# Performance work log

Measured on AMD Instinct MI355X. Metric: run time of the kernel, lower is better.

The kernel has to match this reference:

```python
import jax, jax.numpy as jnp
import numpy as np
from jax import lax

# ---- configuration (matches init_kwargs) ----
B, C_DATA, C_FEAT, H, W = 2, 8, 8, 160, 160
K = 7                      # number of soft nearest neighbors
PS, STRIDE, WIN = 10, 5, 15
FEAT, C_EMB = 64, 8
N1 = (H - PS) // STRIDE + 1   # 31, no padding needed
N2 = (W - PS) // STRIDE + 1   # 31
NEG_INF = -1e9


def _conv3(x, w, b):
    y = lax.conv_general_dilated(x, w, (1, 1), 'SAME',
                                 dimension_numbers=('NCHW', 'OIHW', 'NCHW'))
    return y + b[None, :, None, None]


def _cnn(x, w1, b1, w2, b2, w3, b3):
    # depth-3 DnCNN-style net: conv-relu-conv-relu-conv (bn=False, lastact=linear)
    h = jax.nn.relu(_conv3(x, w1, b1))
    h = jax.nn.relu(_conv3(h, w2, b2))
    return _conv3(h, w3, b3)


def _im2patch(x):
    # x: [b,c,H,W] -> [b,n1,n2,c*PS*PS]; patch flattened channel-major (c,p1,p2)
    ii = jnp.arange(N1)[:, None] * STRIDE + jnp.arange(PS)[None, :]  # [n1,PS]
    jj = jnp.arange(N2)[:, None] * STRIDE + jnp.arange(PS)[None, :]  # [n2,PS]
    p = x[:, :, ii[:, None, :, None], jj[None, :, None, :]]  # [b,c,n1,n2,PS,PS]
    p = jnp.transpose(p, (0, 2, 3, 1, 4, 5))
    return p.reshape(p.shape[0], N1, N2, -1)


def _n3block(x_data, x_faet, ew1, eb1, ew2, eb2, ew3, eb3,
             tw1, tb1, tw2, tb2, tw3, tb3):
    xe = _cnn(x_faet, ew1, eb1, ew2, eb2, ew3, eb3)      # [b,8,H,W] embeddings
    log_temp = _cnn(x_faet, tw1, tb1, tw2, tb2, tw3, tb3)  # [b,1,H,W]

    ye = _im2patch(xe)                        # [b,n1,n2,E]; queries == database
    yp = _im2patch(x_data)                    # [b,n1,n2,F]
    lt = _im2patch(log_temp).mean(-1)         # scalar log-temp per patch
    temp = jnp.exp(lt)[..., None]             # [b,n1,n2,1] (temp_bias = 1)

    S = min(WIN, N1, N2)
    R = S // 2
    base1 = jnp.clip(jnp.arange(N1) - R, 0, N1 - S)   # clamped window top-left
    base2 = jnp.clip(jnp.arange(N2) - R, 0, N2 - S)
    offs = jnp.stack(jnp.meshgrid(jnp.arange(S), jnp.arange(S), indexing='ij'),
                     axis=-1).reshape(-1, 2)          # [S*S,2]
    i1, i2 = jnp.arange(N1), jnp.arange(N2)
    yn = jnp.sum(ye * ye, axis=-1)            # [b,n1,n2] squared norms

    @jax.checkpoint
    def dist_step(carry, off):
        j1 = base1 + off[0]
        j2 = base2 + off[1]
        xs = ye[:, j1][:, :, j2]              # [b,n1,n2,E] candidate embedding
        xn = yn[:, j1][:, :, j2]
        dot = jnp.einsum('bije,bije->bij', ye, xs)
        d = yn + xn - 2.0 * dot               # squared euclidean distance
        self_m = (j1 == i1)[:, None] & (j2 == i2)[None, :]
        return carry, (d, self_m)

    _, (D, selfm) = lax.scan(dist_step, None, offs)
    D = jnp.moveaxis(D, 0, -1)                # [b,n1,n2,O], O=S*S
    selfm = jnp.moveaxis(selfm, 0, -1)        # [n1,n2,O]

    logits = -D / temp
    logits = jnp.where(selfm, NEG_INF, logits)   # exclude_self

    # continuous deterministic top-k (N3Net): w_j = softmax(a); a += log(1 - w_j)
    ws = []
    for _ in range(K):
        wgt = jax.nn.softmax(logits, axis=-1)
        ws.append(wgt)
        logits = logits + jnp.log1p(-jnp.minimum(wgt, 1.0 - 1e-6))
    Wk = jnp.stack(ws, axis=-1)               # [b,n1,n2,O,K]

    @jax.checkpoint
    def agg_step(z, args):
        off, wk = args                        # wk: [b,n1,n2,K]
        j1 = base1 + off[0]
        j2 = base2 + off[1]
        ys = yp[:, j1][:, :, j2]              # [b,n1,n2,F]
        return z + wk[..., :, None] * ys[..., None, :], None

    z0 = jnp.zeros(yp.shape[:3] + (K, yp.shape[-1]), yp.dtype)
    z, _ = lax.scan(agg_step, z0, (offs, jnp.moveaxis(Wk, 3, 0)))
    z = z - yp[..., None, :]                  # residue=True
    out_p = jnp.concatenate([yp[..., None, :], z], axis=3)  # [b,n1,n2,K+1,F]

    # fold patch volumes back to image, averaging overlaps
    b = out_p.shape[0]
    C = (K + 1) * C_DATA
    out_p = out_p.reshape(b, N1, N2, K + 1, C_DATA, PS, PS)
    out_p = jnp.transpose(out_p, (0, 3, 4, 1, 2, 5, 6)).reshape(b, C, N1, N2, PS, PS)
    rows = jnp.arange(N1)[:, None] * STRIDE + jnp.arange(PS)[None, :]
    cols = jnp.arange(N2)[:, None] * STRIDE + jnp.arange(PS)[None, :]
    lin = (rows[:, None, :, None] * W + cols[None, :, None, :]).reshape(-1)
    vals = out_p.reshape(b, C, -1)
    img = jnp.zeros((b, C, H * W), out_p.dtype).at[:, :, lin].add(vals)
    cnt = jnp.zeros((H * W,), out_p.dtype).at[lin].add(1.0)
    return (img / cnt).reshape(b, C, H, W)


def setup_inputs() -> dict:
    key = jax.random.key(0)
    ks = jax.random.split(key, 8)
    f32 = jnp.float32
    wn = lambda k, s: jax.random.normal(k, s, f32) * 0.05
    return dict(
        x_data=jax.random.normal(ks[0], (B, C_DATA, H, W), f32),
        x_faet=jax.random.normal(ks[1], (B, C_FEAT, H, W), f32),
        ew1=wn(ks[2], (FEAT, C_FEAT, 3, 3)), eb1=jnp.zeros((FEAT,), f32),
        ew2=wn(ks[3], (FEAT, FEAT, 3, 3)), eb2=jnp.zeros((FEAT,), f32),
        ew3=wn(ks[4], (C_EMB, FEAT, 3, 3)), eb3=jnp.zeros((C_EMB,), f32),
        tw1=wn(ks[5], (FEAT, C_FEAT, 3, 3)), tb1=jnp.zeros((FEAT,), f32),
        tw2=wn(ks[6], (FEAT, FEAT, 3, 3)), tb2=jnp.zeros((FEAT,), f32),
        tw3=wn(ks[7], (1, FEAT, 3, 3)), tb3=jnp.zeros((1,), f32),
    )


def reference(x_data, x_faet, ew1, eb1, ew2, eb2, ew3, eb3,
              tw1, tb1, tw2, tb2, tw3, tb3):
    return _n3block(x_data, x_faet, ew1, eb1, ew2, eb2, ew3, eb3,
                    tw1, tb1, tw2, tb2, tw3, tb3)
```

## Files before the change

### kernel.cpp

```cpp
#include <hip/hip_runtime.h>
#include <math.h>

#define BN 2
#define HH 160
#define WW 160
#define CDATA 8
#define PS 10
#define STR 5
#define N1 31
#define N2 31
#define NSITE (N1*N2)
#define SITES (BN*NSITE)
#define SWIN 15
#define NOFF 225
#define KK 7
#define EDIM 800
#define NPIX 25600
#define LP 40
#define LP2 72
#define KP 480
#define COLP 992
#define GP 34
#define KSPLIT 5
#define GRAMBLKS (BN*N1*2*KSPLIT)
#define YNTBLKS ((SITES+3)/4)

typedef __attribute__((ext_vector_type(8))) short s8v;
typedef __attribute__((ext_vector_type(8))) unsigned short u8v;
typedef __attribute__((ext_vector_type(4))) unsigned short u4v;
typedef __attribute__((ext_vector_type(4))) float f4v;

__device__ __forceinline__ unsigned short f2bf(float f) {
    unsigned u = __float_as_uint(f);
    return (unsigned short)((u + 0x7FFFu + ((u >> 16) & 1u)) >> 16);
}
__device__ __forceinline__ float bf2f(unsigned short h) {
    return __uint_as_float(((unsigned)h) << 16);
}

__global__ __launch_bounds__(256) void prep_k(const float* __restrict__ ew2,
                                              const float* __restrict__ tw2,
                                              const float* __restrict__ ew1,
                                              const float* __restrict__ tw1,
                                              const float* __restrict__ ew3,
                                              const float* __restrict__ tw3,
                                              unsigned short* __restrict__ wp,
                                              unsigned short* __restrict__ wp1,
                                              unsigned short* __restrict__ wp3) {
    int blk = blockIdx.x;
    int t = threadIdx.x;
    if (blk < 288) {
        int idx = blk * 256 + t;
        int which = idx / (64 * 576); int r = idx % (64 * 576);
        int n = r / 576, k = r % 576;
        int p = k / 64, c = k % 64;
        const float* w = which ? tw2 : ew2;
        wp[idx] = f2bf(w[(n * 64 + c) * 9 + p]);
    } else if (blk < 336) {
        int idx = (blk - 288) * 256 + t;
        if (idx < 128 * 96) {
            int n = idx / 96, k = idx % 96;
            int tap = k >> 3, c = k & 7;
            unsigned short v = 0;
            if (tap < 9) {
                const float* w = (n < 64) ? ew1 : tw1;
                v = f2bf(w[((n & 63) * 8 + c) * 9 + tap]);
            }
            wp1[idx] = v;
        }
    } else {
        int idx = (blk - 336) * 256 + t;
        if (idx < 2 * 16 * 576) {
            int which = idx / (16 * 576); int r = idx % (16 * 576);
            int n = r / 576, k = r % 576;
            int tap = k / 64, c = k % 64;
            float w = 0.f; bool lo = false;
            if (which == 0) { w = ew3[((n & 7) * 64 + c) * 9 + tap]; lo = (n >= 8); }
            else if (n < 2) { w = tw3[c * 9 + tap]; lo = (n == 1); }
            unsigned short hi = f2bf(w);
            wp3[idx] = lo ? f2bf(w - bf2f(hi)) : hi;
            if (which == 1 && n >= 2) wp3[idx] = 0;
        }
    }
}

__global__ __launch_bounds__(256) void conv1_ypt_k(const float* __restrict__ xf,
                                                   const float* __restrict__ xd,
                                                   const unsigned short* __restrict__ wp1,
                                                   const float* __restrict__ eb1,
                                                   const float* __restrict__ tb1,
                                                   unsigned short* __restrict__ h1,
                                                   unsigned short* __restrict__ ypT) {
    const int t = threadIdx.x;
    if (blockIdx.x >= 800) {
        int row = blockIdx.x - 800;
        int b = row / 800, e = row % 800;
        int cd = e & 7, pp = e >> 3;
        int pi = pp / 10, pj = pp % 10;
        const float* src = xd + ((size_t)(b * 8 + cd) * HH + pi) * WW + pj;
        unsigned short* dst = ypT + (size_t)row * COLP;
        for (int it = 0; it < 4; ++it) {
            int col = it * 256 + t;
            if (col < COLP) {
                int j1 = col >> 5, j2 = col & 31;
                unsigned short v = 0;
                if (j2 < 31) v = f2bf(src[(j1 * 5) * WW + j2 * 5]);
                dst[col] = v;
            }
        }
        return;
    }
    __shared__ unsigned short Al[128 * LP];
    __shared__ unsigned short Bl[64 * LP];
    const int m0 = blockIdx.x * 64;
    const int wv = t >> 6, lane = t & 63;
    f4v acc[2][4];
    #pragma unroll
    for (int fj = 0; fj < 2; ++fj)
        #pragma unroll
        for (int fi = 0; fi < 4; ++fi) { f4v z = {0.f,0.f,0.f,0.f}; acc[fj][fi] = z; }
    const int mp = m0 + (t >> 2);
    const int b = mp / NPIX, rp = mp % NPIX;
    const int py = rp / WW, px = rp % WW;
    for (int ks = 0; ks < 3; ++ks) {
        int tap = ks * 4 + (t & 3);
        int dy = tap / 3 - 1, dx = tap % 3 - 1;
        int yy = py + dy, xx = px + dx;
        bool ok = (tap < 9) && yy >= 0 && yy < HH && xx >= 0 && xx < WW;
        u8v bv;
        #pragma unroll
        for (int c = 0; c < 8; ++c)
            bv[c] = ok ? f2bf(xf[((size_t)(b * 8 + c)) * NPIX + yy * WW + xx]) : 0;
        __syncthreads();
        *(u8v*)(Bl + (t >> 2) * LP + (t & 3) * 8) = bv;
        #pragma unroll
        for (int it = 0; it < 2; ++it) {
            int idx = t + it * 256;
            int row = idx >> 2, seg = idx & 3;
            *(u8v*)(Al + row * LP + seg * 8) = *(const u8v*)(wp1 + row * 96 + ks * 32 + seg * 8);
        }
        __syncthreads();
        s8v af[2], bf[4];
        #pragma unroll
        for (int fj = 0; fj < 2; ++fj)
            af[fj] = *(const s8v*)((const short*)Al + (wv * 32 + fj * 16 + (lane & 15)) * LP + (lane >> 4) * 8);
        #pragma unroll
        for (int fi = 0; fi < 4; ++fi)
            bf[fi] = *(const s8v*)((const short*)Bl + (fi * 16 + (lane & 15)) * LP + (lane >> 4) * 8);
        #pragma unroll
        for (int fj = 0; fj < 2; ++fj)
            #pragma unroll
            for (int fi = 0; fi < 4; ++fi)
                acc[fj][fi] = __builtin_amdgcn_mfma_f32_16x16x32_bf16(af[fj], bf[fi], acc[fj][fi], 0, 0, 0);
    }
    #pragma unroll
    for (int fj = 0; fj < 2; ++fj) {
        int nb = wv * 32 + fj * 16 + (lane >> 4) * 4;
        float bias4[4];
        #pragma unroll
        for (int c = 0; c < 4; ++c) {
            int n = nb + c;
            bias4[c] = (n < 64) ? eb1[n] : tb1[n - 64];
        }
        #pragma unroll
        for (int fi = 0; fi < 4; ++fi) {
            int mm = m0 + fi * 16 + (lane & 15);
            ushort4 o;
            o.x = f2bf(fmaxf(acc[fj][fi][0] + bias4[0], 0.f));
            o.y = f2bf(fmaxf(acc[fj][fi][1] + bias4[1], 0.f));
            o.z = f2bf(fmaxf(acc[fj][fi][2] + bias4[2], 0.f));
            o.w = f2bf(fmaxf(acc[fj][fi][3] + bias4[3], 0.f));
            *(ushort4*)(h1 + (size_t)mm * 128 + nb) = o;
        }
    }
}

__global__ __launch_bounds__(256) void conv2_mfma_k(const unsigned short* __restrict__ h1,
                                                    const unsigned short* __restrict__ wp,
                                                    const float* __restrict__ eb2,
                                                    const float* __restrict__ tb2,
                                                    unsigned short* __restrict__ h2) {
    __shared__ unsigned short Al[64 * LP2];
    __shared__ unsigned short Bl[128 * LP2];
    const int t = threadIdx.x;
    const int which = blockIdx.y;
    const int m0 = blockIdx.x * 128;
    const int wv = t >> 6, lane = t & 63;
    f4v acc[4][2];
    #pragma unroll
    for (int nf = 0; nf < 4; ++nf)
        #pragma unroll
        for (int mf = 0; mf < 2; ++mf) { f4v z = {0.f,0.f,0.f,0.f}; acc[nf][mf] = z; }
    const unsigned short* wb = wp + (size_t)which * 64 * 576;
    const int sm = t >> 2, sq = (t & 3) * 8;
    const int mp0 = m0 + sm;
    const int b0 = mp0 / NPIX, rp0 = mp0 % NPIX;
    const int py0 = rp0 / WW, px0 = rp0 % WW;
    const int mp1 = m0 + 64 + sm;
    const int b1_ = mp1 / NPIX, rp1 = mp1 % NPIX;
    const int py1 = rp1 / WW, px1 = rp1 % WW;
    for (int p = 0; p < 9; ++p) {
        const int dy = p / 3 - 1, dx = p % 3 - 1;
        s8v av[2], bv0[2], bv1[2];
        #pragma unroll
        for (int hh = 0; hh < 2; ++hh) {
            av[hh] = *(const s8v*)(wb + sm * 576 + p * 64 + hh * 32 + sq);
            #pragma unroll
            for (int j = 0; j < 8; j++) { bv0[hh][j] = 0; bv1[hh][j] = 0; }
        }
        int yy = py0 + dy, xx = px0 + dx;
        if (yy >= 0 && yy < HH && xx >= 0 && xx < WW) {
            const short* src = (const short*)h1 + ((size_t)b0 * NPIX + yy * WW + xx) * 128 + which * 64 + sq;
            bv0[0] = *(const s8v*)src; bv0[1] = *(const s8v*)(src + 32);
        }
        yy = py1 + dy; xx = px1 + dx;
        if (yy >= 0 && yy < HH && xx >= 0 && xx < WW) {
            const short* src = (const short*)h1 + ((size_t)b1_ * NPIX + yy * WW + xx) * 128 + which * 64 + sq;
            bv1[0] = *(const s8v*)src; bv1[1] = *(const s8v*)(src + 32);
        }
        __syncthreads();
        #pragma unroll
        for (int hh = 0; hh < 2; ++hh) {
            *(s8v*)((short*)Al + sm * LP2 + hh * 32 + sq) = av[hh];
            *(s8v*)((short*)Bl + sm * LP2 + hh * 32 + sq) = bv0[hh];
            *(s8v*)((short*)Bl + (64 + sm) * LP2 + hh * 32 + sq) = bv1[hh];
        }
        __syncthreads();
        #pragma unroll
        for (int kk = 0; kk < 2; ++kk) {
            s8v af[4], bf[2];
            #pragma unroll
            for (int nf = 0; nf < 4; ++nf)
                af[nf] = *(const s8v*)((const short*)Al + (nf * 16 + (lane & 15)) * LP2 + kk * 32 + (lane >> 4) * 8);
            #pragma unroll
            for (int mf = 0; mf < 2; ++mf)
                bf[mf] = *(const s8v*)((const short*)Bl + (wv * 32 + mf * 16 + (lane & 15)) * LP2 + kk * 32 + (lane >> 4) * 8);
            #pragma unroll
            for (int nf = 0; nf < 4; ++nf)
                #pragma unroll
                for (int mf = 0; mf < 2; ++mf)
                    acc[nf][mf] = __builtin_amdgcn_mfma_f32_16x16x32_bf16(af[nf], bf[mf], acc[nf][mf], 0, 0, 0);
        }
    }
    const float* bias = which ? tb2 : eb2;
    #pragma unroll
    for (int nf = 0; nf < 4; ++nf) {
        int nb = nf * 16 + (lane >> 4) * 4;
        f4v bv4 = *(const f4v*)(bias + nb);
        #pragma unroll
        for (int mf = 0; mf < 2; ++mf) {
            int mm = m0 + wv * 32 + mf * 16 + (lane & 15);
            ushort4 o;
            o.x = f2bf(fmaxf(acc[nf][mf][0] + bv4[0], 0.f));
            o.y = f2bf(fmaxf(acc[nf][mf][1] + bv4[1], 0.f));
            o.z = f2bf(fmaxf(acc[nf][mf][2] + bv4[2], 0.f));
            o.w = f2bf(fmaxf(acc[nf][mf][3] + bv4[3], 0.f));
            *(ushort4*)(h2 + ((size_t)which * 51200 + mm) * 64 + nb) = o;
        }
    }
}

__global__ __launch_bounds__(256) void conv3_mfma_k(const unsigned short* __restrict__ h2,
                                                    const unsigned short* __restrict__ wp3,
                                                    const float* __restrict__ eb3,
                                                    const float* __restrict__ tb3,
                                                    unsigned short* __restrict__ xeH,
                                                    unsigned short* __restrict__ xeL,
                                                    float* __restrict__ splane,
                                                    float* __restrict__ ltm) {
    __shared__ unsigned short Al[16 * LP];
    __shared__ unsigned short Bl[128 * LP];
    const int t = threadIdx.x;
    const int which = blockIdx.y;
    const int m0 = blockIdx.x * 128;
    const int wv = t >> 6, lane = t & 63;
    f4v acc[2];
    { f4v z = {0.f,0.f,0.f,0.f}; acc[0] = z; acc[1] = z; }
    const unsigned short* wb = wp3 + (size_t)which * 16 * 576;
    const int sm = t >> 2, sq = (t & 3) * 8;
    const int mp0 = m0 + sm;
    const int b0 = mp0 / NPIX, rp0 = mp0 % NPIX;
    const int py0 = rp0 / WW, px0 = rp0 % WW;
    const int mp1 = m0 + 64 + sm;
    const int b1_ = mp1 / NPIX, rp1 = mp1 % NPIX;
    const int py1 = rp1 / WW, px1 = rp1 % WW;
    for (int step = 0; step < 18; ++step) {
        const int p = step >> 1, ch = (step & 1) * 32;
        const int dy = p / 3 - 1, dx = p % 3 - 1;
        s8v av;
        if (t < 64) av = *(const s8v*)(wb + (t >> 2) * 576 + p * 64 + ch + (t & 3) * 8);
        s8v bv0, bv1;
        #pragma unroll
        for (int j = 0; j < 8; j++) { bv0[j] = 0; bv1[j] = 0; }
        int yy = py0 + dy, xx = px0 + dx;
        if (yy >= 0 && yy < HH && xx >= 0 && xx < WW)
            bv0 = *(const s8v*)((const short*)h2 + ((size_t)which * 51200 + (size_t)b0 * NPIX + yy * WW + xx) * 64 + ch + sq);
        yy = py1 + dy; xx = px1 + dx;
        if (yy >= 0 && yy < HH && xx >= 0 && xx < WW)
            bv1 = *(const s8v*)((const short*)h2 + ((size_t)which * 51200 + (size_t)b1_ * NPIX + yy * WW + xx) * 64 + ch + sq);
        __syncthreads();
        if (t < 64) *(s8v*)((short*)Al + (t >> 2) * LP + (t & 3) * 8) = av;
        *(s8v*)((short*)Bl + sm * LP + sq) = bv0;
        *(s8v*)((short*)Bl + (64 + sm) * LP + sq) = bv1;
        __syncthreads();
        s8v af = *(const s8v*)((const short*)Al + (lane & 15) * LP + (lane >> 4) * 8);
        #pragma unroll
        for (int mf = 0; mf < 2; ++mf) {
            s8v bf = *(const s8v*)((const short*)Bl + (wv * 32 + mf * 16 + (lane & 15)) * LP + (lane >> 4) * 8);
            acc[mf] = __builtin_amdgcn_mfma_f32_16x16x32_bf16(af, bf, acc[mf], 0, 0, 0);
        }
    }
    #pragma unroll
    for (int mf = 0; mf < 2; ++mf) {
        int mm = m0 + wv * 32 + mf * 16 + (lane & 15);
        if (which == 0) {
            f4v hilo;
            #pragma unroll
            for (int c = 0; c < 4; ++c)
                hilo[c] = acc[mf][c] + __shfl_xor(acc[mf][c], 32);
            if (lane < 32) {
                int nb = (lane >> 4) * 4;
                u4v hs, ls;
                float ss = 0.f;
                #pragma unroll
                for (int c = 0; c < 4; ++c) {
                    float v = hilo[c] + eb3[nb + c];
                    unsigned short h = f2bf(v);
                    hs[c] = h;
                    ls[c] = f2bf(v - bf2f(h));
                    ss += v * v;
                }
                *(u4v*)(xeH + (size_t)mm * 8 + nb) = hs;
                *(u4v*)(xeL + (size_t)mm * 8 + nb) = ls;
                ss += __shfl_xor(ss, 16);
                if (lane < 16) splane[mm] = ss;
            }
        } else {
            if ((lane >> 4) == 0)
                ltm[mm] = acc[mf][0] + acc[mf][1] + tb3[0];
        }
    }
}

__global__ __launch_bounds__(256) void gram_ynt_k(const unsigned short* __restrict__ xeH,
                                                  const unsigned short* __restrict__ xeL,
                                                  const float* __restrict__ splane,
                                                  const float* __restrict__ ltm,
                                                  float* __restrict__ dotsC,
                                                  float* __restrict__ yn,
                                                  float* __restrict__ tempv) {
    if (blockIdx.x >= GRAMBLKS) {
        int wv = threadIdx.x >> 6, lane = threadIdx.x & 63;
        int wid = (blockIdx.x - GRAMBLKS) * 4 + wv;
        if (wid >= SITES) return;
        int b = wid / NSITE; int ij = wid % NSITE;
        int i1 = ij / N2, i2 = ij % N2;
        float s1 = 0.f, s2 = 0.f;
        for (int p = lane; p < 100; p += 64) {
            int rr = p / 10, q = p % 10;
            int idx = b * NPIX + (i1 * STR + rr) * WW + i2 * STR + q;
            s1 += splane[idx];
            s2 += ltm[idx];
        }
        #pragma unroll
        for (int o = 32; o; o >>= 1) { s1 += __shfl_xor(s1, o); s2 += __shfl_xor(s2, o); }
        if (lane == 0) {
            yn[wid] = s1;
            tempv[wid] = expf(s2 * (1.f / 100.f));
        }
        return;
    }
    __shared__ unsigned short AsH[32 * GP], AsL[32 * GP];
    __shared__ unsigned short BsH[256 * GP], BsL[256 * GP];
    int blk = blockIdx.x;
    int kc = blk % KSPLIT; int r = blk / KSPLIT;
    int nh = r & 1; r >>= 1;
    int b = r / N1, i1 = r % N1;
    int b1 = min(max(i1 - 7, 0), 16);
    int t = threadIdx.x;
    int wv = t >> 6, lane = t & 63;
    f4v acc[2][4];
    #pragma unroll
    for (int mt = 0; mt < 2; ++mt)
        #pragma unroll
        for (int nt = 0; nt < 4; ++nt) { f4v z = {0.f,0.f,0.f,0.f}; acc[mt][nt] = z; }
    const size_t pbase = (size_t)b * NPIX;
    for (int ks = kc * 5; ks < kc * 5 + 5; ++ks) {
        __syncthreads();
        {
            int idx = t & 127;
            int row = idx >> 2, seg = idx & 3;
            int p = ks * 4 + seg;
            int rr = p / 10, q = p - rr * 10;
            u8v v;
            #pragma unroll
            for (int u = 0; u < 8; ++u) v[u] = 0;
            if (row < 31) {
                size_t a = (pbase + (size_t)(i1 * STR + rr) * WW + row * STR + q) * 8;
                v = *(const u8v*)((t < 128 ? xeH : xeL) + a);
            }
            *(u8v*)((t < 128 ? AsH : AsL) + row * GP + seg * 8) = v;
        }
        #pragma unroll
        for (int rep = 0; rep < 8; ++rep) {
            int idx = t + rep * 256;
            int isH = idx < 1024;
            int id2 = idx & 1023;
            int row = id2 >> 2, seg = id2 & 3;
            int dj = nh * 8 + (row >> 5), j2 = row & 31;
            int p = ks * 4 + seg;
            int rr = p / 10, q = p - rr * 10;
            u8v v;
            #pragma unroll
            for (int u = 0; u < 8; ++u) v[u] = 0;
            if (dj < 15 && j2 < 31) {
                size_t a = (pbase + (size_t)((b1 + dj) * STR + rr) * WW + j2 * STR + q) * 8;
                v = *(const u8v*)((isH ? xeH : xeL) + a);
            }
            *(u8v*)((isH ? BsH : BsL) + row * GP + seg * 8) = v;
        }
        __syncthreads();
        s8v afH[2], afL[2], bfH[4], bfL[4];
        #pragma unroll
        for (int mt = 0; mt < 2; ++mt) {
            int ar = mt * 16 + (lane & 15);
            afH[mt] = *(const s8v*)((const short*)AsH + ar * GP + (lane >> 4) * 8);
            afL[mt] = *(const s8v*)((const short*)AsL + ar * GP + (lane >> 4) * 8);
        }
        #pragma unroll
        for (int nt = 0; nt < 4; ++nt) {
            int br = wv * 64 + nt * 16 + (lane & 15);
            bfH[nt] = *(const s8v*)((const short*)BsH + br * GP + (lane >> 4) * 8);
            bfL[nt] = *(const s8v*)((const short*)BsL + br * GP + (lane >> 4) * 8);
        }
        #pragma unroll
        for (int mt = 0; mt < 2; ++mt)
            #pragma unroll
            for (int nt = 0; nt < 4; ++nt) {
                acc[mt][nt] = __builtin_amdgcn_mfma_f32_16x16x32_bf16(afH[mt], bfH[nt], acc[mt][nt], 0, 0, 0);
                acc[mt][nt] = __builtin_amdgcn_mfma_f32_16x16x32_bf16(afH[mt], bfL[nt], acc[mt][nt], 0, 0, 0);
                acc[mt][nt] = __builtin_amdgcn_mfma_f32_16x16x32_bf16(afL[mt], bfH[nt], acc[mt][nt], 0, 0, 0);
            }
    }
    float* dk = dotsC + (size_t)kc * SITES * NOFF;
    #pragma unroll
    for (int mt = 0; mt < 2; ++mt) {
        int i2b = mt * 16 + (lane >> 4) * 4;
        #pragma unroll
        for (int nt = 0; nt < 4; ++nt) {
            int n = wv * 64 + nt * 16 + (lane & 15);
            int dj = nh * 8 + (n >> 5), j2 = n & 31;
            if (dj >= 15 || j2 >= 31) continue;
            #pragma unroll
            for (int c = 0; c < 4; ++c) {
                int i2 = i2b + c;
                if (i2 >= 31) continue;
                int b2 = min(max(i2 - 7, 0), 16);
                int dc = j2 - b2;
                if (dc < 0 || dc >= SWIN) continue;
                size_t site = (size_t)((b * N1 + i1) * N2 + i2);
                dk[site * NOFF + dj * SWIN + dc] = acc[mt][nt][c];
            }
        }
    }
}

__global__ __launch_bounds__(256) void softmax_awrite_k(const float* __restrict__ dotsC,
                                                        const float* __restrict__ yn,
                                                        const float* __restrict__ tempv,
                                                        unsigned short* __restrict__ Aglob) {
    __shared__ float sw[4][228];
    int wv = threadIdx.x >> 6, lane = threadIdx.x & 63;
    int wid = blockIdx.x * 4 + wv;
    bool active = (wid < SITES);
    int wids = active ? wid : (SITES - 1);
    int b = wids / NSITE; int ij = wids % NSITE;
    int i1 = ij / N2, i2 = ij % N2;
    int b1 = min(max(i1 - 7, 0), 16);
    int b2 = min(max(i2 - 7, 0), 16);
    int pglob = i2 >> 1, s = i2 & 1;
    unsigned short* Abase = Aglob + (size_t)((b * N1 + i1) * 256) * KP;
    float yns = yn[wids];
    float tvi = 1.f / tempv[wids];
    float lg[4];
    #pragma unroll
    for (int r = 0; r < 4; ++r) {
        int t = lane + 64 * r;
        lg[r] = -1e9f;
        if (t < NOFF) {
            float dot = 0.f;
            #pragma unroll
            for (int kc = 0; kc < KSPLIT; ++kc)
                dot += dotsC[((size_t)kc * SITES + wids) * NOFF + t];
            int dj = t / SWIN, dc = t % SWIN;
            int j1 = b1 + dj, j2 = b2 + dc;
            float xn = yn[(b * N1 + j1) * N2 + j2];
            float d = yns + xn - 2.f * dot;
            lg[r] = -d * tvi;
            if (j1 == i1 && j2 == i2) lg[r] = -1e9f;
        }
    }
    for (int k = 0; k < KK; ++k) {
        float m = fmaxf(fmaxf(lg[0], lg[1]), fmaxf(lg[2], lg[3]));
        #pragma unroll
        for (int o = 32; o; o >>= 1) m = fmaxf(m, __shfl_xor(m, o));
        float ex[4]; float ssum = 0.f;
        #pragma unroll
        for (int r = 0; r < 4; ++r) { ex[r] = __expf(lg[r] - m); ssum += ex[r]; }
        #pragma unroll
        for (int o = 32; o; o >>= 1) ssum += __shfl_xor(ssum, o);
        float inv = 1.f / ssum;
        #pragma unroll
        for (int r = 0; r < 4; ++r) {
            float wgt = ex[r] * inv;
            int t = lane + 64 * r;
            if (t < NOFF) sw[wv][t] = wgt;
            lg[r] += log1pf(-fminf(wgt, 1.f - 1e-6f));
        }
        __syncthreads();
        if (active && lane < 60) {
            u8v o;
            #pragma unroll
            for (int u = 0; u < 8; ++u) {
                int n = lane * 8 + u;
                int dj = n >> 5, j2 = n & 31;
                int dc = j2 - b2;
                o[u] = (j2 < 31 && dc >= 0 && dc < SWIN) ? f2bf(sw[wv][dj * SWIN + dc]) : (unsigned short)0;
            }
            int m_ = 16 * pglob + k + 7 * s;
            *(u8v*)(Abase + (size_t)m_ * KP + lane * 8) = o;
        }
        __syncthreads();
    }
    if (active && s == 0 && lane < 60) {
        u8v z;
        #pragma unroll
        for (int u = 0; u < 8; ++u) z[u] = 0;
        *(u8v*)(Abase + (size_t)(16 * pglob + 14) * KP + lane * 8) = z;
        *(u8v*)(Abase + (size_t)(16 * pglob + 15) * KP + lane * 8) = z;
        if (i2 == 30) {
            #pragma unroll
            for (int sl = 7; sl < 14; ++sl)
                *(u8v*)(Abase + (size_t)(16 * 15 + sl) * KP + lane * 8) = z;
        }
    }
}

__global__ __launch_bounds__(256) void agg_gemm_k(const unsigned short* __restrict__ Aglob,
                                                  const unsigned short* __restrict__ ypT,
                                                  unsigned short* __restrict__ zbuf) {
    __shared__ unsigned short As[128 * 40];
    __shared__ unsigned short Bs[160 * 40];
    int blk = blockIdx.x;
    int b = blk / 310; int r = blk % 310;
    int i1 = r / 10; int r2 = r % 10;
    int mh = r2 / 5, nc = r2 % 5;
    int b1 = min(max(i1 - 7, 0), 16);
    int t = threadIdx.x;
    int wv = t >> 6, lane = t & 63;
    int wm = (wv & 1) * 64, we = (wv >> 1) * 80;
    const unsigned short* Ab = Aglob + ((size_t)(b * N1 + i1) * 256 + mh * 128) * KP;
    const unsigned short* Bb = ypT + ((size_t)b * 800 + nc * 160) * COLP + b1 * 32;
    f4v accr[4][5];
    #pragma unroll
    for (int mt = 0; mt < 4; ++mt)
        #pragma unroll
        for (int et = 0; et < 5; ++et) { f4v z = {0.f,0.f,0.f,0.f}; accr[mt][et] = z; }
    for (int ks = 0; ks < 15; ++ks) {
        __syncthreads();
        #pragma unroll
        for (int it = 0; it < 2; ++it) {
            int idx = t + it * 256;
            int row = idx >> 2, seg = idx & 3;
            *(u8v*)(As + row * 40 + seg * 8) = *(const u8v*)(Ab + (size_t)row * KP + ks * 32 + seg * 8);
        }
        #pragma unroll
        for (int it = 0; it < 3; ++it) {
            int idx = t + it * 256;
            if (idx < 640) {
                int row = idx >> 2, seg = idx & 3;
                *(u8v*)(Bs + row * 40 + seg * 8) = *(const u8v*)(Bb + (size_t)row * COLP + ks * 32 + seg * 8);
            }
        }
        __syncthreads();
        s8v af[4], bf[5];
        #pragma unroll
        for (int mt = 0; mt < 4; ++mt)
            af[mt] = *(const s8v*)((const short*)As + (wm + mt * 16 + (lane & 15)) * 40 + (lane >> 4) * 8);
        #pragma unroll
        for (int et = 0; et < 5; ++et)
            bf[et] = *(const s8v*)((const short*)Bs + (we + et * 16 + (lane & 15)) * 40 + (lane >> 4) * 8);
        #pragma unroll
        for (int mt = 0; mt < 4; ++mt)
            #pragma unroll
            for (int et = 0; et < 5; ++et)
                accr[mt][et] = __builtin_amdgcn_mfma_f32_16x16x32_bf16(af[mt], bf[et], accr[mt][et], 0, 0, 0);
    }
    unsigned short* zb = zbuf + ((size_t)(b * N1 + i1) * 256 + mh * 128) * 800 + nc * 160;
    #pragma unroll
    for (int mt = 0; mt < 4; ++mt) {
        int mrow = wm + mt * 16 + (lane >> 4) * 4;
        #pragma unroll
        for (int et = 0; et < 5; ++et) {
            int ecol = we + et * 16 + (lane & 15);
            #pragma unroll
            for (int c = 0; c < 4; ++c)
                zb[(size_t)(mrow + c) * 800 + ecol] = f2bf(accr[mt][et][c]);
        }
    }
}

__global__ __launch_bounds__(256) void finalize_k(const unsigned short* __restrict__ zbuf,
                                                  const float* __restrict__ xd,
                                                  float* __restrict__ out) {
    int pid = blockIdx.x * 256 + threadIdx.x;
    if (pid >= BN * NPIX) return;
    int b = pid / NPIX, pix = pid % NPIX;
    int h = pix / WW, w_ = pix % WW;
    int lo1 = max(0, (h - 5) / 5),  hi1 = min(30, h / 5);
    int lo2 = max(0, (w_ - 5) / 5), hi2 = min(30, w_ / 5);
    float cntinv = 1.f / (float)((hi1 - lo1 + 1) * (hi2 - lo2 + 1));
    float xv[8];
    #pragma unroll
    for (int cd = 0; cd < 8; ++cd) {
        xv[cd] = xd[((size_t)(b * 8 + cd)) * NPIX + pix];
        out[((size_t)(b * 64 + cd)) * NPIX + pix] = xv[cd];
    }
    for (int k = 0; k < KK; ++k) {
        float s[8];
        #pragma unroll
        for (int cd = 0; cd < 8; ++cd) s[cd] = 0.f;
        for (int i1 = lo1; i1 <= hi1; ++i1) {
            int pi = h - 5 * i1;
            for (int i2 = lo2; i2 <= hi2; ++i2) {
                int pj = w_ - 5 * i2;
                int m = 16 * (i2 >> 1) + k + 7 * (i2 & 1);
                const unsigned short* zp = zbuf + ((size_t)(b * N1 + i1) * 256 + m) * 800 + (pi * 10 + pj) * 8;
                u8v zv = *(const u8v*)zp;
                #pragma unroll
                for (int cd = 0; cd < 8; ++cd) s[cd] += bf2f(zv[cd]);
            }
        }
        #pragma unroll
        for (int cd = 0; cd < 8; ++cd)
            out[((size_t)(b * 64 + (k + 1) * 8 + cd)) * NPIX + pix] = s[cd] * cntinv - xv[cd];
    }
}

extern "C" void kernel_launch(void* const* d_in, const int* in_sizes, int n_in,
                              void* d_out, int out_size, void* d_ws, size_t ws_size,
                              hipStream_t stream) {
    (void)in_sizes; (void)n_in; (void)out_size; (void)ws_size;
    const float* x_data = (const float*)d_in[0];
    const float* x_faet = (const float*)d_in[1];
    const float* ew1 = (const float*)d_in[2];  const float* eb1 = (const float*)d_in[3];
    const float* ew2 = (const float*)d_in[4];  const float* eb2 = (const float*)d_in[5];
    const float* ew3 = (const float*)d_in[6];  const float* eb3 = (const float*)d_in[7];
    const float* tw1 = (const float*)d_in[8];  const float* tb1 = (const float*)d_in[9];
    const float* tw2 = (const float*)d_in[10]; const float* tb2 = (const float*)d_in[11];
    const float* tw3 = (const float*)d_in[12]; const float* tb3 = (const float*)d_in[13];
    float* out = (float*)d_out;

    char* base = (char*)d_ws;
    unsigned short* h1 = (unsigned short*)(base);
    unsigned short* h2 = (unsigned short*)(base + 13107200);
    unsigned short* wp1 = (unsigned short*)(base + 13107200);
    unsigned short* wp = (unsigned short*)(base + 26214400);
    float* yn    = (float*)(base + 26361856);
    float* tempv = (float*)(base + 26370048);
    unsigned short* ypT = (unsigned short*)(base + 26378240);
    unsigned short* xeH = (unsigned short*)(base + 29552640);
    unsigned short* xeL = (unsigned short*)(base + 30371840);
    float* ltm    = (float*)(base + 31191040);
    float* splane = (float*)(base + 31395840);
    unsigned short* wp3 = (unsigned short*)(base + 37546240);
    unsigned short* Aglob = (unsigned short*)(base + 29552640);
    float* dotsC = (float*)h2;
    unsigned short* zbuf = (unsigned short*)base;

    prep_k<<<408, 256, 0, stream>>>(ew2, tw2, ew1, tw1, ew3, tw3, wp, wp1, wp3);
    conv1_ypt_k<<<800 + 1600, 256, 0, stream>>>(x_faet, x_data, wp1, eb1, tb1, h1, ypT);
    conv2_mfma_k<<<dim3(400, 2), 256, 0, stream>>>(h1, wp, eb2, tb2, h2);
    conv3_mfma_k<<<dim3(400, 2), 256, 0, stream>>>(h2, wp3, eb3, tb3, xeH, xeL, splane, ltm);

    gram_ynt_k<<<GRAMBLKS + YNTBLKS, 256, 0, stream>>>(xeH, xeL, splane, ltm, dotsC, yn, tempv);
    softmax_awrite_k<<<YNTBLKS, 256, 0, stream>>>(dotsC, yn, tempv, Aglob);

    agg_gemm_k<<<BN * 310, 256, 0, stream>>>(Aglob, ypT, zbuf);
    finalize_k<<<(BN * NPIX + 255) / 256, 256, 0, stream>>>(zbuf, x_data, out);
}
```

Measured before the change: 159.1 us.

## Load MFMA operands directly from global memory, dropping LDS staging in GEMM kernels

Four MFMA kernels (conv2, conv3, gram, aggregation GEMM) stop staging A/B tiles through shared memory with __syncthreads barriers. Each lane now loads its fragment straight from global memory in MFMA operand layout, with boundary checks turned into predicated zero fills. This removes LDS round-trips and barrier stalls. In exchange, data shared across waves is fetched redundantly from global/L2, and the per-lane 16-byte loads are less coalesced.

```diff
diff --git a/kernel.cpp b/kernel.cpp
--- a/kernel.cpp
+++ b/kernel.cpp
@@ -17,10 +17,8 @@
 #define EDIM 800
 #define NPIX 25600
 #define LP 40
-#define LP2 72
 #define KP 480
 #define COLP 992
-#define GP 34
 #define KSPLIT 5
 #define GRAMBLKS (BN*N1*2*KSPLIT)
 #define YNTBLKS ((SITES+3)/4)
@@ -36,6 +34,12 @@
 }
 __device__ __forceinline__ float bf2f(unsigned short h) {
     return __uint_as_float(((unsigned)h) << 16);
+}
+__device__ __forceinline__ s8v zero8() {
+    s8v v;
+    #pragma unroll
+    for (int j = 0; j < 8; ++j) v[j] = 0;
+    return v;
 }
 
 __global__ __launch_bounds__(256) void prep_k(const float* __restrict__ ew2,
@@ -180,67 +184,50 @@
                                                     const float* __restrict__ eb2,
                                                     const float* __restrict__ tb2,
                                                     unsigned short* __restrict__ h2) {
-    __shared__ unsigned short Al[64 * LP2];
-    __shared__ unsigned short Bl[128 * LP2];
     const int t = threadIdx.x;
     const int which = blockIdx.y;
     const int m0 = blockIdx.x * 128;
     const int wv = t >> 6, lane = t & 63;
+    const int seg = (lane >> 4) * 8;
+    const unsigned short* wb = wp + (size_t)which * 64 * 576;
+    int pyv[2], pxv[2]; size_t pb[2];
+    #pragma unroll
+    for (int mf = 0; mf < 2; ++mf) {
+        int mp = m0 + wv * 32 + mf * 16 + (lane & 15);
+        int b = mp / NPIX, rp = mp % NPIX;
+        pyv[mf] = rp / WW; pxv[mf] = rp % WW;
+        pb[mf] = (size_t)b * NPIX;
+    }
     f4v acc[4][2];
     #pragma unroll
     for (int nf = 0; nf < 4; ++nf)
         #pragma unroll
         for (int mf = 0; mf < 2; ++mf) { f4v z = {0.f,0.f,0.f,0.f}; acc[nf][mf] = z; }
-    const unsigned short* wb = wp + (size_t)which * 64 * 576;
-    const int sm = t >> 2, sq = (t & 3) * 8;
-    const int mp0 = m0 + sm;
-    const int b0 = mp0 / NPIX, rp0 = mp0 % NPIX;
-    const int py0 = rp0 / WW, px0 = rp0 % WW;
-    const int mp1 = m0 + 64 + sm;
-    const int b1_ = mp1 / NPIX, rp1 = mp1 % NPIX;
-    const int py1 = rp1 / WW, px1 = rp1 % WW;
     for (int p = 0; p < 9; ++p) {
         const int dy = p / 3 - 1, dx = p % 3 - 1;
-        s8v av[2], bv0[2], bv1[2];
-        #pragma unroll
-        for (int hh = 0; hh < 2; ++hh) {
-            av[hh] = *(const s8v*)(wb + sm * 576 + p * 64 + hh * 32 + sq);
-            #pragma unroll
-            for (int j = 0; j < 8; j++) { bv0[hh][j] = 0; bv1[hh][j] = 0; }
-        }
-        int yy = py0 + dy, xx = px0 + dx;
-        if (yy >= 0 && yy < HH && xx >= 0 && xx < WW) {
-            const short* src = (const short*)h1 + ((size_t)b0 * NPIX + yy * WW + xx) * 128 + which * 64 + sq;
-            bv0[0] = *(const s8v*)src; bv0[1] = *(const s8v*)(src + 32);
-        }
-        yy = py1 + dy; xx = px1 + dx;
-        if (yy >= 0 && yy < HH && xx >= 0 && xx < WW) {
-            const short* src = (const short*)h1 + ((size_t)b1_ * NPIX + yy * WW + xx) * 128 + which * 64 + sq;
-            bv1[0] = *(const s8v*)src; bv1[1] = *(const s8v*)(src + 32);
-        }
-        __syncthreads();
-        #pragma unroll
-        for (int hh = 0; hh < 2; ++hh) {
-            *(s8v*)((short*)Al + sm * LP2 + hh * 32 + sq) = av[hh];
-            *(s8v*)((short*)Bl + sm * LP2 + hh * 32 + sq) = bv0[hh];
-            *(s8v*)((short*)Bl + (64 + sm) * LP2 + hh * 32 + sq) = bv1[hh];
-        }
-        __syncthreads();
-        #pragma unroll
-        for (int kk = 0; kk < 2; ++kk) {
-            s8v af[4], bf[2];
-            #pragma unroll
-            for (int nf = 0; nf < 4; ++nf)
-                af[nf] = *(const s8v*)((const short*)Al + (nf * 16 + (lane & 15)) * LP2 + kk * 32 + (lane >> 4) * 8);
-            #pragma unroll
-            for (int mf = 0; mf < 2; ++mf)
-                bf[mf] = *(const s8v*)((const short*)Bl + (wv * 32 + mf * 16 + (lane & 15)) * LP2 + kk * 32 + (lane >> 4) * 8);
+        s8v af[4][2];
+        #pragma unroll
+        for (int nf = 0; nf < 4; ++nf)
+            #pragma unroll
+            for (int kk = 0; kk < 2; ++kk)
+                af[nf][kk] = *(const s8v*)(wb + (nf * 16 + (lane & 15)) * 576 + p * 64 + kk * 32 + seg);
+        s8v bf[2][2];
+        #pragma unroll
+        for (int mf = 0; mf < 2; ++mf) {
+            int yy = pyv[mf] + dy, xx = pxv[mf] + dx;
+            bool ok = (yy >= 0 && yy < HH && xx >= 0 && xx < WW);
+            const short* src = (const short*)h1 + (pb[mf] + (size_t)(ok ? yy * WW + xx : 0)) * 128 + which * 64 + seg;
+            #pragma unroll
+            for (int kk = 0; kk < 2; ++kk)
+                bf[mf][kk] = ok ? *(const s8v*)(src + kk * 32) : zero8();
+        }
+        #pragma unroll
+        for (int kk = 0; kk < 2; ++kk)
             #pragma unroll
             for (int nf = 0; nf < 4; ++nf)
                 #pragma unroll
                 for (int mf = 0; mf < 2; ++mf)
-                    acc[nf][mf] = __builtin_amdgcn_mfma_f32_16x16x32_bf16(af[nf], bf[mf], acc[nf][mf], 0, 0, 0);
-        }
+                    acc[nf][mf] = __builtin_amdgcn_mfma_f32_16x16x32_bf16(af[nf][kk], bf[mf][kk], acc[nf][mf], 0, 0, 0);
     }
     const float* bias = which ? tb2 : eb2;
     #pragma unroll
@@ -268,45 +255,32 @@
                                                     unsigned short* __restrict__ xeL,
                                                     float* __restrict__ splane,
                                                     float* __restrict__ ltm) {
-    __shared__ unsigned short Al[16 * LP];
-    __shared__ unsigned short Bl[128 * LP];
     const int t = threadIdx.x;
     const int which = blockIdx.y;
     const int m0 = blockIdx.x * 128;
     const int wv = t >> 6, lane = t & 63;
+    const int seg = (lane >> 4) * 8;
+    const unsigned short* wb = wp3 + (size_t)which * 16 * 576;
+    int pyv[2], pxv[2]; size_t pb[2];
+    #pragma unroll
+    for (int mf = 0; mf < 2; ++mf) {
+        int mp = m0 + wv * 32 + mf * 16 + (lane & 15);
+        int b = mp / NPIX, rp = mp % NPIX;
+        pyv[mf] = rp / WW; pxv[mf] = rp % WW;
+        pb[mf] = (size_t)which * 51200 + (size_t)b * NPIX;
+    }
     f4v acc[2];
     { f4v z = {0.f,0.f,0.f,0.f}; acc[0] = z; acc[1] = z; }
-    const unsigned short* wb = wp3 + (size_t)which * 16 * 576;
-    const int sm = t >> 2, sq = (t & 3) * 8;
-    const int mp0 = m0 + sm;
-    const int b0 = mp0 / NPIX, rp0 = mp0 % NPIX;
-    const int py0 = rp0 / WW, px0 = rp0 % WW;
-    const int mp1 = m0 + 64 + sm;
-    const int b1_ = mp1 / NPIX, rp1 = mp1 % NPIX;
-    const int py1 = rp1 / WW, px1 = rp1 % WW;
     for (int step = 0; step < 18; ++step) {
         const int p = step >> 1, ch = (step & 1) * 32;
         const int dy = p / 3 - 1, dx = p % 3 - 1;
-        s8v av;
-        if (t < 64) av = *(const s8v*)(wb + (t >> 2) * 576 + p * 64 + ch + (t & 3) * 8);
-        s8v bv0, bv1;
-        #pragma unroll
-        for (int j = 0; j < 8; j++) { bv0[j] = 0; bv1[j] = 0; }
-        int yy = py0 + dy, xx = px0 + dx;
-        if (yy >= 0 && yy < HH && xx >= 0 && xx < WW)
-            bv0 = *(const s8v*)((const short*)h2 + ((size_t)which * 51200 + (size_t)b0 * NPIX + yy * WW + xx) * 64 + ch + sq);
-        yy = py1 + dy; xx = px1 + dx;
-        if (yy >= 0 && yy < HH && xx >= 0 && xx < WW)
-            bv1 = *(const s8v*)((const short*)h2 + ((size_t)which * 51200 + (size_t)b1_ * NPIX + yy * WW + xx) * 64 + ch + sq);
-        __syncthreads();
-        if (t < 64) *(s8v*)((short*)Al + (t >> 2) * LP + (t & 3) * 8) = av;
-        *(s8v*)((short*)Bl + sm * LP + sq) = bv0;
-        *(s8v*)((short*)Bl + (64 + sm) * LP + sq) = bv1;
-        __syncthreads();
-        s8v af = *(const s8v*)((const short*)Al + (lane & 15) * LP + (lane >> 4) * 8);
+        s8v af = *(const s8v*)(wb + (lane & 15) * 576 + p * 64 + ch + seg);
         #pragma unroll
         for (int mf = 0; mf < 2; ++mf) {
-            s8v bf = *(const s8v*)((const short*)Bl + (wv * 32 + mf * 16 + (lane & 15)) * LP + (lane >> 4) * 8);
+            int yy = pyv[mf] + dy, xx = pxv[mf] + dx;
+            bool ok = (yy >= 0 && yy < HH && xx >= 0 && xx < WW);
+            s8v bf = ok ? *(const s8v*)((const short*)h2 + (pb[mf] + (size_t)(yy * WW + xx)) * 64 + ch + seg)
+                        : zero8();
             acc[mf] = __builtin_amdgcn_mfma_f32_16x16x32_bf16(af, bf, acc[mf], 0, 0, 0);
         }
     }
@@ -370,8 +344,6 @@
         }
         return;
     }
-    __shared__ unsigned short AsH[32 * GP], AsL[32 * GP];
-    __shared__ unsigned short BsH[256 * GP], BsL[256 * GP];
     int blk = blockIdx.x;
     int kc = blk % KSPLIT; int r = blk / KSPLIT;
     int nh = r & 1; r >>= 1;
@@ -385,53 +357,30 @@
         #pragma unroll
         for (int nt = 0; nt < 4; ++nt) { f4v z = {0.f,0.f,0.f,0.f}; acc[mt][nt] = z; }
     const size_t pbase = (size_t)b * NPIX;
+    int brj[4], brd[4]; bool bok[4];
+    #pragma unroll
+    for (int nt = 0; nt < 4; ++nt) {
+        int br = wv * 64 + nt * 16 + (lane & 15);
+        brd[nt] = nh * 8 + (br >> 5); brj[nt] = br & 31;
+        bok[nt] = (brd[nt] < 15) && (brj[nt] < 31);
+    }
     for (int ks = kc * 5; ks < kc * 5 + 5; ++ks) {
-        __syncthreads();
-        {
-            int idx = t & 127;
-            int row = idx >> 2, seg = idx & 3;
-            int p = ks * 4 + seg;
-            int rr = p / 10, q = p - rr * 10;
-            u8v v;
-            #pragma unroll
-            for (int u = 0; u < 8; ++u) v[u] = 0;
-            if (row < 31) {
-                size_t a = (pbase + (size_t)(i1 * STR + rr) * WW + row * STR + q) * 8;
-                v = *(const u8v*)((t < 128 ? xeH : xeL) + a);
-            }
-            *(u8v*)((t < 128 ? AsH : AsL) + row * GP + seg * 8) = v;
-        }
-        #pragma unroll
-        for (int rep = 0; rep < 8; ++rep) {
-            int idx = t + rep * 256;
-            int isH = idx < 1024;
-            int id2 = idx & 1023;
-            int row = id2 >> 2, seg = id2 & 3;
-            int dj = nh * 8 + (row >> 5), j2 = row & 31;
-            int p = ks * 4 + seg;
-            int rr = p / 10, q = p - rr * 10;
-            u8v v;
-            #pragma unroll
-            for (int u = 0; u < 8; ++u) v[u] = 0;
-            if (dj < 15 && j2 < 31) {
-                size_t a = (pbase + (size_t)((b1 + dj) * STR + rr) * WW + j2 * STR + q) * 8;
-                v = *(const u8v*)((isH ? xeH : xeL) + a);
-            }
-            *(u8v*)((isH ? BsH : BsL) + row * GP + seg * 8) = v;
-        }
-        __syncthreads();
+        int p4 = ks * 4 + (lane >> 4);
+        int rr = p4 / 10, q = p4 - rr * 10;
         s8v afH[2], afL[2], bfH[4], bfL[4];
         #pragma unroll
         for (int mt = 0; mt < 2; ++mt) {
             int ar = mt * 16 + (lane & 15);
-            afH[mt] = *(const s8v*)((const short*)AsH + ar * GP + (lane >> 4) * 8);
-            afL[mt] = *(const s8v*)((const short*)AsL + ar * GP + (lane >> 4) * 8);
+            bool ok = (ar < 31);
+            size_t a = (pbase + (size_t)(i1 * STR + rr) * WW + (ok ? ar : 0) * STR + q) * 8;
+            afH[mt] = ok ? *(const s8v*)(xeH + a) : zero8();
+            afL[mt] = ok ? *(const s8v*)(xeL + a) : zero8();
         }
         #pragma unroll
         for (int nt = 0; nt < 4; ++nt) {
-            int br = wv * 64 + nt * 16 + (lane & 15);
-            bfH[nt] = *(const s8v*)((const short*)BsH + br * GP + (lane >> 4) * 8);
-            bfL[nt] = *(const s8v*)((const short*)BsL + br * GP + (lane >> 4) * 8);
+            size_t a = (pbase + (size_t)((b1 + (bok[nt] ? brd[nt] : 0)) * STR + rr) * WW + (bok[nt] ? brj[nt] : 0) * STR + q) * 8;
+            bfH[nt] = bok[nt] ? *(const s8v*)(xeH + a) : zero8();
+            bfL[nt] = bok[nt] ? *(const s8v*)(xeL + a) : zero8();
         }
         #pragma unroll
         for (int mt = 0; mt < 2; ++mt)
@@ -549,8 +498,6 @@
 __global__ __launch_bounds__(256) void agg_gemm_k(const unsigned short* __restrict__ Aglob,
                                                   const unsigned short* __restrict__ ypT,
                                                   unsigned short* __restrict__ zbuf) {
-    __shared__ unsigned short As[128 * 40];
-    __shared__ unsigned short Bs[160 * 40];
     int blk = blockIdx.x;
     int b = blk / 310; int r = blk % 310;
     int i1 = r / 10; int r2 = r % 10;
@@ -559,6 +506,7 @@
     int t = threadIdx.x;
     int wv = t >> 6, lane = t & 63;
     int wm = (wv & 1) * 64, we = (wv >> 1) * 80;
+    const int seg = (lane >> 4) * 8;
     const unsigned short* Ab = Aglob + ((size_t)(b * N1 + i1) * 256 + mh * 128) * KP;
     const unsigned short* Bb = ypT + ((size_t)b * 800 + nc * 160) * COLP + b1 * 32;
     f4v accr[4][5];
@@ -567,29 +515,13 @@
         #pragma unroll
         for (int et = 0; et < 5; ++et) { f4v z = {0.f,0.f,0.f,0.f}; accr[mt][et] = z; }
     for (int ks = 0; ks < 15; ++ks) {
-        __syncthreads();
-        #pragma unroll
-        for (int it = 0; it < 2; ++it) {
-            int idx = t + it * 256;
-            int row = idx >> 2, seg = idx & 3;
-            *(u8v*)(As + row * 40 + seg * 8) = *(const u8v*)(Ab + (size_t)row * KP + ks * 32 + seg * 8);
-        }
-        #pragma unroll
-        for (int it = 0; it < 3; ++it) {
-            int idx = t + it * 256;
-            if (idx < 640) {
-                int row = idx >> 2, seg = idx & 3;
-                *(u8v*)(Bs + row * 40 + seg * 8) = *(const u8v*)(Bb + (size_t)row * COLP + ks * 32 + seg * 8);
-            }
-        }
-        __syncthreads();
         s8v af[4], bf[5];
         #pragma unroll
         for (int mt = 0; mt < 4; ++mt)
-            af[mt] = *(const s8v*)((const short*)As + (wm + mt * 16 + (lane & 15)) * 40 + (lane >> 4) * 8);
+            af[mt] = *(const s8v*)(Ab + (size_t)(wm + mt * 16 + (lane & 15)) * KP + ks * 32 + seg);
         #pragma unroll
         for (int et = 0; et < 5; ++et)
-            bf[et] = *(const s8v*)((const short*)Bs + (we + et * 16 + (lane & 15)) * 40 + (lane >> 4) * 8);
+            bf[et] = *(const s8v*)(Bb + (size_t)(we + et * 16 + (lane & 15)) * COLP + ks * 32 + seg);
         #pragma unroll
         for (int mt = 0; mt < 4; ++mt)
             #pragma unroll
```

New measurement: 201.7 us. 1.27x slower.
